# Optimization experiments

Hardware: AMD Instinct MI355X
Metric: run time of the kernel (lower is better)

## Reference

```python
import jax, jax.numpy as jnp
import numpy as np

SEG_SIZES = list(range(3, 102, 2))   # 50 segment sizes, as in FractalImage.__init__
BETA = 4.0                            # soft-count sigmoid sharpness
EPS = 1e-8
R_CAP = 20                            # max number of radii per segment size


def _segment(x, k):
    # Non-overlapping k x k patches: (B,H,W) -> (B, P, k*k)
    B, H, W = x.shape
    nh, nw = H // k, W // k
    p = x[:, :nh * k, :nw * k].reshape(B, nh, k, nw, k)
    return p.transpose(0, 1, 3, 2, 4).reshape(B, nh * nw, k * k)


def _metric_feats(d, radii):
    # d: (B,P,K2) distances from patch center; radii: (R,)
    soft = jax.nn.sigmoid((radii - d[..., None]) * BETA)   # (B,P,K2,R) soft indicator d<=r
    n = soft.mean(axis=2)                                  # (B,P,R) per-patch filling fraction
    nbar = n.mean(axis=1)                                  # (B,R)
    lx = jnp.log(radii)
    xc = lx - lx.mean()
    slope = (jnp.log(nbar + EPS) * xc).sum(-1) / (xc * xc).sum()
    fd = -slope                                            # (B,) fractal dimension
    m1 = n.mean(axis=1)                                    # (B,R) first moment over patches
    m2 = (n * n).mean(axis=1)                              # (B,R) second moment
    lac = (m2 / (m1 * m1 + EPS)).mean(axis=-1)             # (B,) lacunarity
    return fd, lac


def _features_k(x, k):
    patches = _segment(x, k)                               # (B,P,K2)
    c = k // 2
    center = patches[:, :, c * k + c][..., None]
    di = jnp.abs(patches - center)                         # intensity distance to center
    ii, jj = np.meshgrid(np.arange(k), np.arange(k), indexing='ij')
    dy = jnp.asarray(np.abs(ii - c).reshape(-1), jnp.float32)   # (K2,)
    dx = jnp.asarray(np.abs(jj - c).reshape(-1), jnp.float32)   # (K2,)
    R = int(min(max((k - 1) // 2, 2), R_CAP))
    radii = jnp.arange(1, R + 1, dtype=jnp.float32)
    d_cheb = jnp.maximum(jnp.maximum(dy, dx), di)
    d_euc = jnp.sqrt(dy * dy + dx * dx + di * di)
    d_man = dy + dx + di
    return tuple(_metric_feats(d, radii) for d in (d_cheb, d_euc, d_man))


def _forward(x):
    # one pass per segment size (fixed python loop over 50 static sizes)
    feats = [jax.checkpoint(lambda xx, kk=k: _features_k(xx, kk))(x) for k in SEG_SIZES]
    channels = []
    for m in range(3):  # Chebyshev, Euclidean, Manhattan
        fd = jnp.stack([f[m][0] for f in feats], axis=0)   # (50,B)
        lac = jnp.stack([f[m][1] for f in feats], axis=0)  # (50,B)
        # AssembleChannel: transpose, concat [lac, fd] -> (B,100) -> (B,10,10)
        ch = jnp.concatenate([lac.T, fd.T], axis=1).reshape(-1, 10, 10)
        channels.append(ch)
    # AssembleImage: stack metrics as channels -> (B,10,10,3)
    return jnp.stack(channels, axis=-1)


def setup_inputs() -> dict:
    key = jax.random.key(0)
    x = jax.random.uniform(key, (16, 224, 224), dtype=jnp.float32)
    return {"x": x}


def reference(x):
    return _forward(x)
```

## Files before the change

kernel.cpp:

```cpp
#include <hip/hip_runtime.h>
#include <stdint.h>


#define L2E4f 5.770780163555854f
#define QE4f  0.0183156388887342f

struct Tabs {
  int gpre[51];
  int CH[50];
  int kofseq[50];
  int GT;
  int eoff[18], ecnt[18];
  int moff[18], mcnt[18];
  int pbase;
};

__device__ __constant__ float LXT[20] = {
  0.0f, 0.69314718f, 1.09861229f, 1.38629436f, 1.60943791f,
  1.79175947f, 1.94591015f, 2.07944154f, 2.19722458f, 2.30258509f,
  2.39789527f, 2.48490665f, 2.56494936f, 2.63905733f, 2.70805020f,
  2.77258872f, 2.83321334f, 2.89037176f, 2.94443898f, 2.99573227f};

constexpr float PRt[21] = {1.0f,
  5.45981500e1f, 2.98095799e3f, 1.62754791e5f, 8.88611052e6f, 4.85165195e8f,
  2.64891221e10f, 1.44625706e12f, 7.89629602e13f, 4.31123155e15f, 2.35385267e17f,
  1.28516001e19f, 7.01673591e20f, 3.83100800e22f, 2.09165950e24f, 1.14200739e26f,
  6.23514908e27f, 3.40427605e29f, 1.85867175e31f, 1.01480039e33f, 5.54062238e34f};
constexpr float QRt[21] = {1.0f,
  1.83156389e-2f, 3.35462628e-4f, 6.14421235e-6f, 1.12535175e-7f, 2.06115362e-9f,
  3.77513454e-11f, 6.91440011e-13f, 1.26641655e-14f, 2.31952283e-16f, 4.24835426e-18f,
  7.78113224e-20f, 1.42516408e-21f, 2.61027907e-23f, 4.78089288e-25f, 8.75651076e-27f,
  1.60381089e-28f, 2.93748211e-30f, 5.38018616e-32f, 9.85415469e-34f, 1.80485139e-35f};

__device__ __forceinline__ float wred64(float v) {
#pragma unroll
  for (int off = 32; off > 0; off >>= 1) v += __shfl_xor(v, off, 64);
  return v;
}

__device__ __forceinline__ int csqrt_d(int v) {
  if (v <= 0) return 0;
  int x = (int)sqrtf((float)v);
  while (x * x < v) ++x;
  while (x > 0 && (x - 1) * (x - 1) >= v) --x;
  return x;
}

__global__ __launch_bounds__(256) void build_lists(uint32_t* ws, Tabs tab) {
  const int ci = (int)blockIdx.x >> 1;
  const int metric = (int)blockIdx.x & 1;
  const int c_eff = 8 + ci;
  const int cb = (c_eff < 24) ? c_eff : 24;
  const int Rcl = (c_eff < 20) ? c_eff : 20;
  const int tid = (int)threadIdx.x;

  if (metric == 1) {
    const int t1 = (Rcl + 4 < 24) ? Rcl + 4 : 24;
    const int smax = (t1 < 2 * cb) ? t1 : 2 * cb;
    uint32_t* dst = ws + tab.moff[ci];
    for (int s = tid; s <= smax; s += 256) {
      int off = 0;
      for (int s2 = 0; s2 < s; ++s2)
        off += (s2 == 0) ? 1 : ((s2 <= cb) ? 4 * s2 : ((s2 <= 2 * cb) ? 4 * (2 * cb - s2 + 1) : 0));
      const int lim = (s < cb) ? s : cb;
      for (int iy = -lim; iy <= lim; ++iy) {
        const int v = s - ((iy >= 0) ? iy : -iy);
        if (v > cb) continue;
        const uint32_t hs = ((uint32_t)s << 16) | ((uint32_t)(iy + 32) << 8);
        if (v == 0) dst[off++] = hs | 32u;
        else { dst[off++] = hs | (uint32_t)(-v + 32); dst[off++] = hs | (uint32_t)(v + 32); }
      }
    }
    if (tid == 0) {
      int total = 0;
      for (int s = 0; s <= smax; ++s)
        total += (s == 0) ? 1 : ((s <= cb) ? 4 * s : ((s <= 2 * cb) ? 4 * (2 * cb - s + 1) : 0));
      const uint32_t dummy = (40u << 16) | ((uint32_t)(cb + 32) << 8) | (uint32_t)(cb + 32);
      for (int q = total; q < tab.mcnt[ci]; ++q) dst[q] = dummy;
    }
  } else {
    const int amax = (Rcl + 4 < 24) ? Rcl + 4 : 24;
    const int W = 2 * cb + 1;
    __shared__ int rs[25 * 49];
    __shared__ int abase[26];
    uint32_t* dst = ws + tab.eoff[ci];
    for (int pid = tid; pid < (amax + 1) * W; pid += 256) {
      const int a = pid / W, iy = pid % W - cb;
      const int B = (a + 1) * (a + 1) - iy * iy;
      int len = 0;
      if (B > 0) {
        const int A = a * a - iy * iy;
        const int x0 = csqrt_d(A);
        int x1 = csqrt_d(B); if (x1 > cb + 1) x1 = cb + 1;
        if (x1 > x0) len = (x0 == 0) ? (2 * x1 - 1) : 2 * (x1 - x0);
      }
      rs[pid] = len;
    }
    __syncthreads();
    if (tid <= amax) {
      int acc = 0;
      for (int iyi = 0; iyi < W; ++iyi) { const int L = rs[tid * W + iyi]; rs[tid * W + iyi] = acc; acc += L; }
      abase[tid + 1] = acc;
    }
    __syncthreads();
    if (tid == 0) { abase[0] = 0; for (int a = 1; a <= amax + 1; ++a) abase[a] += abase[a - 1]; }
    __syncthreads();
    for (int pid = tid; pid < (amax + 1) * W; pid += 256) {
      const int a = pid / W, iy = pid % W - cb;
      const int B = (a + 1) * (a + 1) - iy * iy;
      if (B <= 0) continue;
      const int A = a * a - iy * iy;
      const int x0 = csqrt_d(A);
      int x1 = csqrt_d(B); if (x1 > cb + 1) x1 = cb + 1;
      if (x1 <= x0) continue;
      int off = abase[a] + rs[pid];
      const uint32_t hs = ((uint32_t)a << 16) | ((uint32_t)(iy + 32) << 8);
      if (x0 == 0) {
        for (int dx = -(x1 - 1); dx <= x1 - 1; ++dx) dst[off++] = hs | (uint32_t)(dx + 32);
      } else {
        for (int dx = -(x1 - 1); dx <= -x0; ++dx) dst[off++] = hs | (uint32_t)(dx + 32);
        for (int dx = x0; dx <= x1 - 1; ++dx)     dst[off++] = hs | (uint32_t)(dx + 32);
      }
    }
    __syncthreads();
    if (tid == 0) {
      const int total = abase[amax + 1];
      const uint32_t dummy = (40u << 16) | ((uint32_t)(cb + 32) << 8) | (uint32_t)(cb + 32);
      for (int q = total; q < tab.ecnt[ci]; ++q) dst[q] = dummy;
    }
  }
}

template<int MAXR>
__device__ __forceinline__ void subwave_path(
    const float* __restrict__ xb, float (*s_red)[80],
    int k, int c, int nw, int k2, int R, float invk2, float rcpk,
    int pstart, int pend, int ch, int lpl, int wid, int lane) {
  const int LP = 1 << lpl;
  const int grp = lane >> lpl;
  const int l0 = lane & (LP - 1);
  const int gpw = 64 >> lpl;
  const int conc = gpw << 2;
  const int rounds = (ch + conc - 1) / conc;

  for (int it = 0; it < rounds; ++it) {
    const int patch = pstart + it * conc + wid * gpw + grp;
    float av[2][MAXR];
#pragma unroll
    for (int m = 0; m < 2; ++m)
#pragma unroll
      for (int r = 0; r < MAXR; ++r) av[m][r] = 0.0f;

    if (patch < pend) {
      const int ph = patch / nw, pw = patch - ph * nw;
      const float* pb = xb + (ph * k) * 224 + pw * k;
      const float center = pb[c * 224 + c];
      for (int p = l0; p < k2; p += LP) {
        const int i = (int)(((float)p + 0.5f) * rcpk);
        const int j = p - i * k;
        const float dy = fabsf((float)(i - c));
        const float dx = fabsf((float)(j - c));
        const float di = fabsf(pb[i * 224 + j] - center);
        const float dman = dy + dx + di;
        const float deuc = sqrtf(dy * dy + dx * dx + di * di);
        float Ee = __builtin_amdgcn_exp2f(L2E4f * (deuc - 1.0f));
        float Em = __builtin_amdgcn_exp2f(L2E4f * (dman - 1.0f));
#pragma unroll
        for (int r = 0; r < MAXR; ++r) {
          if (r < R) {
            av[0][r] += __builtin_amdgcn_rcpf(1.0f + Ee);
            av[1][r] += __builtin_amdgcn_rcpf(1.0f + Em);
            Ee *= QE4f; Em *= QE4f;
          }
        }
      }
    }
#pragma unroll
    for (int m = 0; m < 2; ++m)
#pragma unroll
      for (int r = 0; r < MAXR; ++r) {
        if (r < R) {
          float t = av[m][r];
          for (int off = LP >> 1; off > 0; off >>= 1) t += __shfl_xor(t, off, 64);
          float n = t * invk2;
          float nn = n * n;
          for (int off = LP; off < 64; off <<= 1) {
            n += __shfl_xor(n, off, 64);
            nn += __shfl_xor(nn, off, 64);
          }
          if (lane == 0) {
            s_red[wid][m * 40 + r * 2] += n;
            s_red[wid][m * 40 + r * 2 + 1] += nn;
          }
        }
      }
  }
}

template<int METRIC>
__device__ __forceinline__ void list_pass_pair(
    const uint32_t* __restrict__ lst, int pairs,
    const float* __restrict__ pb, float center,
    int c, int R, float (&av)[2][20], int lane) {
  uint32_t e0 = lst[lane];
  uint32_t e1 = lst[64 + lane];
  for (int it = 0; it < pairs; ++it) {
    const int iy0 = (int)((e0 >> 8) & 255) - 32, dx0 = (int)(e0 & 255) - 32;
    const int iy1 = (int)((e1 >> 8) & 255) - 32, dx1 = (int)(e1 & 255) - 32;
    const float px0 = pb[(c + iy0) * 224 + (c + dx0)];
    const float px1 = pb[(c + iy1) * 224 + (c + dx1)];
    const int s0 = (int)(e0 >> 16), s1 = (int)(e1 >> 16);
    const int slo = __builtin_amdgcn_readfirstlane(s0);
    const int shi = __builtin_amdgcn_readfirstlane(__shfl(s1, 63));
    uint32_t en0 = 0u, en1 = 0u;
    if (it + 1 < pairs) {
      en0 = lst[(2 * it + 2) * 64 + lane];
      en1 = lst[(2 * it + 3) * 64 + lane];
    }

    const int rlo = (slo - 2 > 1) ? slo - 2 : 1;
    const float di0 = fabsf(px0 - center);
    const float di1 = fabsf(px1 - center);
    float d0, d1;
    if (METRIC == 1) {
      d0 = (float)s0 + di0;
      d1 = (float)s1 + di1;
    } else {
      d0 = sqrtf(fmaf(di0, di0, (float)(iy0 * iy0 + dx0 * dx0)));
      d1 = sqrtf(fmaf(di1, di1, (float)(iy1 * iy1 + dx1 * dx1)));
    }
    const float g0 = __builtin_amdgcn_exp2f(-L2E4f * d0);
    const float g1 = __builtin_amdgcn_exp2f(-L2E4f * d1);
    const float gs = g0 + g1;
    float E0 = __builtin_amdgcn_exp2f(L2E4f * (d0 - (float)rlo));
    float E1 = __builtin_amdgcn_exp2f(L2E4f * (d1 - (float)rlo));
    const bool haveones = (shi + 4 <= R);
    const float hs = haveones
        ? (__builtin_amdgcn_rcpf(g0) + __builtin_amdgcn_rcpf(g1)) : 0.0f;
#pragma unroll
    for (int r = 1; r <= 20; ++r) {
      if (r <= R) {
        if (r < rlo) {
          av[METRIC][r - 1] = fmaf(PRt[r], gs, av[METRIC][r - 1]);
        } else if (r <= shi + 3) {
          av[METRIC][r - 1] += __builtin_amdgcn_rcpf(1.0f + E0)
                             + __builtin_amdgcn_rcpf(1.0f + E1);
          E0 *= QE4f; E1 *= QE4f;
        } else {
          av[METRIC][r - 1] += fmaf(hs, -QRt[r], 2.0f);
        }
      }
    }
    e0 = en0; e1 = en1;
  }
}

__global__ __launch_bounds__(256) void fractal_main(const float* __restrict__ x,
                                                    float* __restrict__ ws, Tabs tab) {
  const int g = (int)blockIdx.x;
  const int b = (int)blockIdx.y;
  int seq = 0;
  while (g >= tab.gpre[seq + 1]) ++seq;
  const int kidx = tab.kofseq[seq];
  const int lc = g - tab.gpre[seq];
  const int k = 3 + 2 * kidx, c = k >> 1, nw = 224 / k;
  const int P = nw * nw, k2 = k * k;
  int R = kidx + 1; if (R < 2) R = 2; if (R > 20) R = 20;
  const float invk2 = 1.0f / (float)k2;
  const float rcpk = 1.0f / (float)k;
  const float* xb = x + b * 50176;
  const int tid = (int)threadIdx.x, wid = tid >> 6, lane = tid & 63;
  const int ch = tab.CH[kidx];
  const int pstart = lc * ch;
  int pend = pstart + ch; if (pend > P) pend = P;

  __shared__ float s_red[4][80];
  for (int t = tid; t < 320; t += 256) (&s_red[0][0])[t] = 0.0f;
  __syncthreads();

  if (kidx <= 6) {
    const int lpl = (kidx <= 2) ? 0 : 2;
    subwave_path<8>(xb, s_red, k, c, nw, k2, R, invk2, rcpk, pstart, pend, ch, lpl, wid, lane);
  } else {
    const int ci = (kidx + 1 <= 24) ? (kidx - 7) : 17;
    const uint32_t* wsu = (const uint32_t*)ws;
    const uint32_t* el = wsu + tab.eoff[ci];
    const uint32_t* ml = wsu + tab.moff[ci];
    const int ep = tab.ecnt[ci] >> 7, mp = tab.mcnt[ci] >> 7;
    for (int patch = pstart + wid; patch < pend; patch += 4) {
      const int ph = patch / nw, pw = patch - ph * nw;
      const float* pb = xb + (ph * k) * 224 + pw * k;
      const float center = pb[c * 224 + c];
      float av[2][20];
#pragma unroll
      for (int m = 0; m < 2; ++m)
#pragma unroll
        for (int r = 0; r < 20; ++r) av[m][r] = 0.0f;

      list_pass_pair<0>(el, ep, pb, center, c, R, av, lane);
      list_pass_pair<1>(ml, mp, pb, center, c, R, av, lane);

#pragma unroll
      for (int m = 0; m < 2; ++m)
#pragma unroll
        for (int r = 0; r < 20; ++r) {
          if (r < R) {
            const float tot = wred64(av[m][r]);
            if (lane == 0) {
              const float n = tot * invk2;
              s_red[wid][m * 40 + r * 2] += n;
              s_red[wid][m * 40 + r * 2 + 1] += n * n;
            }
          }
        }
    }
  }

  __syncthreads();
  float* dst = ws + tab.pbase + ((size_t)b * tab.GT + g) * 80;
  if (tid < 80) dst[tid] = s_red[0][tid] + s_red[1][tid] + s_red[2][tid] + s_red[3][tid];
}

__global__ __launch_bounds__(64) void fractal_final(const float* __restrict__ ws,
                                                    float* __restrict__ out, Tabs tab) {
  const int kb = (int)blockIdx.x;
  const int kidx = kb >> 4, b = kb & 15;
  int seq = 0;
  for (int j = 0; j < 50; ++j) if (tab.kofseq[j] == kidx) seq = j;
  const int g0 = tab.gpre[seq], g1 = tab.gpre[seq + 1];
  const int k = 3 + 2 * kidx, c = k >> 1, nw = 224 / k;
  const int P = nw * nw, k2 = k * k;
  int R = kidx + 1; if (R < 2) R = 2; if (R > 20) R = 20;
  const float invP = 1.0f / (float)P;
  const int lane = (int)threadIdx.x;

  float lmean = 0.0f;
  for (int r0 = 0; r0 < 20; ++r0) if (r0 < R) lmean += LXT[r0];
  lmean /= (float)R;
  float sxx = 0.0f;
  for (int r0 = 0; r0 < 20; ++r0)
    if (r0 < R) { const float xc = LXT[r0] - lmean; sxx += xc * xc; }

  __shared__ float s_lac[64], s_sxy[64];
  float lact = 0.0f, sxyt = 0.0f;
  if (lane < 60) {
    const int mo = lane / 20;
    const int r0 = lane % 20, rr = r0 + 1;
    if (rr <= R) {
      float m1, m2;
      if (mo == 0) {
        int s0 = rr - 3; if (s0 > c) s0 = c;
        float acc = (s0 >= 0) ? (1.0f + 4.0f * (float)(s0 * (s0 + 1))) : 0.0f;
        int slo = rr - 2; if (slo < 0) slo = 0;
        int shi = rr + 3; if (shi > c) shi = c;
        for (int s = slo; s <= shi; ++s) {
          const float w = (s == 0) ? 1.0f : 8.0f * (float)s;
          acc += w * __builtin_amdgcn_rcpf(
                   1.0f + __builtin_amdgcn_exp2f(L2E4f * (float)(s - rr)));
        }
        m1 = acc / (float)k2;
        m2 = m1 * m1;
      } else {
        const int mws = mo - 1;
        float sn = 0.0f, sn2 = 0.0f;
        for (int gg = g0; gg < g1; ++gg) {
          const float* p = ws + tab.pbase + ((size_t)b * tab.GT + gg) * 80 + mws * 40 + r0 * 2;
          sn += p[0]; sn2 += p[1];
        }
        m1 = sn * invP; m2 = sn2 * invP;
      }
      lact = m2 / (m1 * m1 + 1e-8f);
      sxyt = logf(m1 + 1e-8f) * (LXT[r0] - lmean);
    }
  }
  s_lac[lane] = lact; s_sxy[lane] = sxyt;
  __syncthreads();
  if (lane < 3) {
    float L = 0.0f, S = 0.0f;
    for (int r0 = 0; r0 < 20; ++r0) { L += s_lac[lane * 20 + r0]; S += s_sxy[lane * 20 + r0]; }
    out[b * 300 + kidx * 3 + lane] = L / (float)R;
    out[b * 300 + (50 + kidx) * 3 + lane] = -S / sxx;
  }
}

static inline int csqrt_h(int v) {
  if (v <= 0) return 0;
  int x = 0;
  while (x * x < v) ++x;
  return x;
}

extern "C" void kernel_launch(void* const* d_in, const int* in_sizes, int n_in,
                              void* d_out, int out_size, void* d_ws, size_t ws_size,
                              hipStream_t stream) {
  Tabs tab;

  int lw = 0;
  for (int ci = 0; ci < 18; ++ci) {
    const int c_eff = 8 + ci;
    const int cb = (c_eff < 24) ? c_eff : 24;
    const int Rcl = (c_eff < 20) ? c_eff : 20;
    const int amax = (Rcl + 4 < 24) ? Rcl + 4 : 24;
    const int t1 = (Rcl + 4 < 24) ? Rcl + 4 : 24;
    const int smax = (t1 < 2 * cb) ? t1 : 2 * cb;
    int ec = 0;
    for (int a = 0; a <= amax; ++a)
      for (int iy = -cb; iy <= cb; ++iy) {
        const int B = (a + 1) * (a + 1) - iy * iy;
        if (B <= 0) continue;
        const int A = a * a - iy * iy;
        const int x0 = csqrt_h(A);
        int x1 = csqrt_h(B); if (x1 > cb + 1) x1 = cb + 1;
        if (x1 > x0) ec += (x0 == 0) ? (2 * x1 - 1) : 2 * (x1 - x0);
      }
    int mc = 0;
    for (int s = 0; s <= smax; ++s)
      mc += (s == 0) ? 1 : ((s <= cb) ? 4 * s : ((s <= 2 * cb) ? 4 * (2 * cb - s + 1) : 0));
    const int ecp = (ec + 127) & ~127;
    const int mcp = (mc + 127) & ~127;
    tab.eoff[ci] = lw; tab.ecnt[ci] = ecp; lw += ecp;
    tab.moff[ci] = lw; tab.mcnt[ci] = mcp; lw += mcp;
  }
  tab.pbase = lw;
  const long budget = (long)ws_size - 4L * lw;

  long T = 10000;
  int G_[50], CH_[50];
  long bc[50];
  for (int tries = 0; tries < 8; ++tries) {
    long GTl = 0;
    for (int i = 0; i < 50; ++i) {
      const int k = 3 + 2 * i, nw = 224 / k, P = nw * nw, k2 = k * k;
      int R = i + 1; if (R < 2) R = 2; if (R > 20) R = 20;
      if (i <= 6) {
        const int lpl = (i <= 2) ? 0 : 2;
        const int LP = 1 << lpl, conc = 256 >> lpl;
        const long rc = (long)((k2 + LP - 1) / LP) * 2L * (12L * R + 8L);
        long np = T / rc; if (np < 1) np = 1;
        long cht = np * conc; if (cht > P) cht = P;
        int G = (int)(((long)P + cht - 1) / cht);
        int ch = (P + G - 1) / G; G = (P + ch - 1) / ch;
        G_[i] = G; CH_[i] = ch;
        bc[i] = (long)((ch + conc - 1) / conc) * rc;
      } else {
        const int ci = (i + 1 <= 24) ? (i - 7) : 17;
        const long trips = (long)((tab.ecnt[ci] + tab.mcnt[ci]) >> 6);
        const long ppc = trips * 340 + 1100;
        long nppb = T / ppc; if (nppb < 4) nppb = 4;
        int cht = (int)(((nppb + 3) / 4) * 4); if (cht > P) cht = P;
        int G = (P + cht - 1) / cht;
        int ch = (P + G - 1) / G; G = (P + ch - 1) / ch;
        G_[i] = G; CH_[i] = ch;
        bc[i] = (long)((ch + 3) / 4) * ppc;
      }
      GTl += G_[i];
    }
    if (16L * GTl * 80L * 4L <= budget || tries == 7) break;
    T *= 2;
  }
  int ord[50];
  for (int i = 0; i < 50; ++i) ord[i] = i;
  for (int a = 1; a < 50; ++a) {
    const int key = ord[a]; const long kw = bc[key];
    int bp = a - 1;
    while (bp >= 0 && bc[ord[bp]] < kw) { ord[bp + 1] = ord[bp]; --bp; }
    ord[bp + 1] = key;
  }
  tab.gpre[0] = 0;
  for (int j = 0; j < 50; ++j) {
    tab.kofseq[j] = ord[j];
    tab.gpre[j + 1] = tab.gpre[j] + G_[ord[j]];
  }
  for (int i = 0; i < 50; ++i) tab.CH[i] = CH_[i];
  tab.GT = tab.gpre[50];

  const float* x = (const float*)d_in[0];
  build_lists<<<36, 256, 0, stream>>>((uint32_t*)d_ws, tab);
  fractal_main<<<dim3(tab.GT, 16), 256, 0, stream>>>(x, (float*)d_ws, tab);
  fractal_final<<<800, 64, 0, stream>>>((const float*)d_ws, (float*)d_out, tab);
}
```

Measured before the change: 185.5 us.

## Process two patches per wave in list pass to amortize offset decode

The list-driven path for larger segment sizes now has each wave handle two adjacent patches at once. Offset decode, list loads and readfirstlane work are shared, and there is twice the independent transcendental work for latency hiding. The transition window is narrowed by one radius (rlo uses slo-1, the exact band ends at shi+2), so fewer exact sigmoid evaluations are done. The host work-cost model and chunk rounding are retuned for the 8-patch-per-block stride. Register pressure rises with two accumulator arrays, and the narrower band may change accuracy.

```diff
diff --git a/kernel.cpp b/kernel.cpp
--- a/kernel.cpp
+++ b/kernel.cpp
@@ -198,17 +198,20 @@
 }
 
 template<int METRIC>
-__device__ __forceinline__ void list_pass_pair(
+__device__ __forceinline__ void list_pass_dual(
     const uint32_t* __restrict__ lst, int pairs,
-    const float* __restrict__ pb, float center,
-    int c, int R, float (&av)[2][20], int lane) {
+    const float* __restrict__ pbA, float cenA,
+    const float* __restrict__ pbB, float cenB,
+    int c, int R, float (&avA)[20], float (&avB)[20], int lane) {
   uint32_t e0 = lst[lane];
   uint32_t e1 = lst[64 + lane];
   for (int it = 0; it < pairs; ++it) {
     const int iy0 = (int)((e0 >> 8) & 255) - 32, dx0 = (int)(e0 & 255) - 32;
     const int iy1 = (int)((e1 >> 8) & 255) - 32, dx1 = (int)(e1 & 255) - 32;
-    const float px0 = pb[(c + iy0) * 224 + (c + dx0)];
-    const float px1 = pb[(c + iy1) * 224 + (c + dx1)];
+    const int off0 = (c + iy0) * 224 + (c + dx0);
+    const int off1 = (c + iy1) * 224 + (c + dx1);
+    const float pA0 = pbA[off0], pA1 = pbA[off1];
+    const float pB0 = pbB[off0], pB1 = pbB[off1];
     const int s0 = (int)(e0 >> 16), s1 = (int)(e1 >> 16);
     const int slo = __builtin_amdgcn_readfirstlane(s0);
     const int shi = __builtin_amdgcn_readfirstlane(__shfl(s1, 63));
@@ -218,36 +221,49 @@
       en1 = lst[(2 * it + 3) * 64 + lane];
     }
 
-    const int rlo = (slo - 2 > 1) ? slo - 2 : 1;
-    const float di0 = fabsf(px0 - center);
-    const float di1 = fabsf(px1 - center);
-    float d0, d1;
+    const int rlo = (slo - 1 > 1) ? slo - 1 : 1;
+    const float diA0 = fabsf(pA0 - cenA), diA1 = fabsf(pA1 - cenA);
+    const float diB0 = fabsf(pB0 - cenB), diB1 = fabsf(pB1 - cenB);
+    float dA0, dA1, dB0, dB1;
     if (METRIC == 1) {
-      d0 = (float)s0 + di0;
-      d1 = (float)s1 + di1;
+      dA0 = (float)s0 + diA0; dA1 = (float)s1 + diA1;
+      dB0 = (float)s0 + diB0; dB1 = (float)s1 + diB1;
     } else {
-      d0 = sqrtf(fmaf(di0, di0, (float)(iy0 * iy0 + dx0 * dx0)));
-      d1 = sqrtf(fmaf(di1, di1, (float)(iy1 * iy1 + dx1 * dx1)));
-    }
-    const float g0 = __builtin_amdgcn_exp2f(-L2E4f * d0);
-    const float g1 = __builtin_amdgcn_exp2f(-L2E4f * d1);
-    const float gs = g0 + g1;
-    float E0 = __builtin_amdgcn_exp2f(L2E4f * (d0 - (float)rlo));
-    float E1 = __builtin_amdgcn_exp2f(L2E4f * (d1 - (float)rlo));
-    const bool haveones = (shi + 4 <= R);
-    const float hs = haveones
-        ? (__builtin_amdgcn_rcpf(g0) + __builtin_amdgcn_rcpf(g1)) : 0.0f;
+      const float rho0 = (float)(iy0 * iy0 + dx0 * dx0);
+      const float rho1 = (float)(iy1 * iy1 + dx1 * dx1);
+      dA0 = sqrtf(fmaf(diA0, diA0, rho0)); dA1 = sqrtf(fmaf(diA1, diA1, rho1));
+      dB0 = sqrtf(fmaf(diB0, diB0, rho0)); dB1 = sqrtf(fmaf(diB1, diB1, rho1));
+    }
+    const float gA0 = __builtin_amdgcn_exp2f(-L2E4f * dA0);
+    const float gA1 = __builtin_amdgcn_exp2f(-L2E4f * dA1);
+    const float gB0 = __builtin_amdgcn_exp2f(-L2E4f * dB0);
+    const float gB1 = __builtin_amdgcn_exp2f(-L2E4f * dB1);
+    const float gsA = gA0 + gA1, gsB = gB0 + gB1;
+    float EA0 = __builtin_amdgcn_exp2f(L2E4f * (dA0 - (float)rlo));
+    float EA1 = __builtin_amdgcn_exp2f(L2E4f * (dA1 - (float)rlo));
+    float EB0 = __builtin_amdgcn_exp2f(L2E4f * (dB0 - (float)rlo));
+    float EB1 = __builtin_amdgcn_exp2f(L2E4f * (dB1 - (float)rlo));
+    const bool haveones = (shi + 3 <= R);
+    float hsA = 0.0f, hsB = 0.0f;
+    if (haveones) {
+      hsA = __builtin_amdgcn_rcpf(gA0) + __builtin_amdgcn_rcpf(gA1);
+      hsB = __builtin_amdgcn_rcpf(gB0) + __builtin_amdgcn_rcpf(gB1);
+    }
 #pragma unroll
     for (int r = 1; r <= 20; ++r) {
       if (r <= R) {
         if (r < rlo) {
-          av[METRIC][r - 1] = fmaf(PRt[r], gs, av[METRIC][r - 1]);
-        } else if (r <= shi + 3) {
-          av[METRIC][r - 1] += __builtin_amdgcn_rcpf(1.0f + E0)
-                             + __builtin_amdgcn_rcpf(1.0f + E1);
-          E0 *= QE4f; E1 *= QE4f;
+          avA[r - 1] = fmaf(PRt[r], gsA, avA[r - 1]);
+          avB[r - 1] = fmaf(PRt[r], gsB, avB[r - 1]);
+        } else if (r <= shi + 2) {
+          avA[r - 1] += __builtin_amdgcn_rcpf(1.0f + EA0)
+                      + __builtin_amdgcn_rcpf(1.0f + EA1);
+          avB[r - 1] += __builtin_amdgcn_rcpf(1.0f + EB0)
+                      + __builtin_amdgcn_rcpf(1.0f + EB1);
+          EA0 *= QE4f; EA1 *= QE4f; EB0 *= QE4f; EB1 *= QE4f;
         } else {
-          av[METRIC][r - 1] += fmaf(hs, -QRt[r], 2.0f);
+          avA[r - 1] += fmaf(hsA, -QRt[r], 2.0f);
+          avB[r - 1] += fmaf(hsB, -QRt[r], 2.0f);
         }
       }
     }
@@ -287,32 +303,57 @@
     const uint32_t* el = wsu + tab.eoff[ci];
     const uint32_t* ml = wsu + tab.moff[ci];
     const int ep = tab.ecnt[ci] >> 7, mp = tab.mcnt[ci] >> 7;
-    for (int patch = pstart + wid; patch < pend; patch += 4) {
-      const int ph = patch / nw, pw = patch - ph * nw;
-      const float* pb = xb + (ph * k) * 224 + pw * k;
-      const float center = pb[c * 224 + c];
-      float av[2][20];
-#pragma unroll
-      for (int m = 0; m < 2; ++m)
-#pragma unroll
-        for (int r = 0; r < 20; ++r) av[m][r] = 0.0f;
-
-      list_pass_pair<0>(el, ep, pb, center, c, R, av, lane);
-      list_pass_pair<1>(ml, mp, pb, center, c, R, av, lane);
-
-#pragma unroll
-      for (int m = 0; m < 2; ++m)
-#pragma unroll
-        for (int r = 0; r < 20; ++r) {
-          if (r < R) {
-            const float tot = wred64(av[m][r]);
-            if (lane == 0) {
-              const float n = tot * invk2;
-              s_red[wid][m * 40 + r * 2] += n;
-              s_red[wid][m * 40 + r * 2 + 1] += n * n;
+    for (int patch = pstart + wid * 2; patch < pend; patch += 8) {
+      const bool hasB = (patch + 1 < pend);
+      const int pbi = hasB ? patch + 1 : patch;
+      const int phA = patch / nw, pwA = patch - phA * nw;
+      const int phB = pbi / nw,  pwB = pbi - phB * nw;
+      const float* pbA = xb + (phA * k) * 224 + pwA * k;
+      const float* pbB = xb + (phB * k) * 224 + pwB * k;
+      const float cenA = pbA[c * 224 + c];
+      const float cenB = pbB[c * 224 + c];
+
+      float avA[20], avB[20];
+#pragma unroll
+      for (int r = 0; r < 20; ++r) { avA[r] = 0.0f; avB[r] = 0.0f; }
+      list_pass_dual<0>(el, ep, pbA, cenA, pbB, cenB, c, R, avA, avB, lane);
+#pragma unroll
+      for (int r = 0; r < 20; ++r) {
+        if (r < R) {
+          const float ta = wred64(avA[r]);
+          const float tb = wred64(avB[r]);
+          if (lane == 0) {
+            const float na = ta * invk2;
+            s_red[wid][r * 2] += na;
+            s_red[wid][r * 2 + 1] += na * na;
+            if (hasB) {
+              const float nb = tb * invk2;
+              s_red[wid][r * 2] += nb;
+              s_red[wid][r * 2 + 1] += nb * nb;
             }
           }
         }
+      }
+#pragma unroll
+      for (int r = 0; r < 20; ++r) { avA[r] = 0.0f; avB[r] = 0.0f; }
+      list_pass_dual<1>(ml, mp, pbA, cenA, pbB, cenB, c, R, avA, avB, lane);
+#pragma unroll
+      for (int r = 0; r < 20; ++r) {
+        if (r < R) {
+          const float ta = wred64(avA[r]);
+          const float tb = wred64(avB[r]);
+          if (lane == 0) {
+            const float na = ta * invk2;
+            s_red[wid][40 + r * 2] += na;
+            s_red[wid][40 + r * 2 + 1] += na * na;
+            if (hasB) {
+              const float nb = tb * invk2;
+              s_red[wid][40 + r * 2] += nb;
+              s_red[wid][40 + r * 2 + 1] += nb * nb;
+            }
+          }
+        }
+      }
     }
   }
 
@@ -445,13 +486,13 @@
       } else {
         const int ci = (i + 1 <= 24) ? (i - 7) : 17;
         const long trips = (long)((tab.ecnt[ci] + tab.mcnt[ci]) >> 6);
-        const long ppc = trips * 340 + 1100;
-        long nppb = T / ppc; if (nppb < 4) nppb = 4;
-        int cht = (int)(((nppb + 3) / 4) * 4); if (cht > P) cht = P;
+        const long ppc = trips * 250 + 1100;
+        long nppb = T / ppc; if (nppb < 8) nppb = 8;
+        int cht = (int)(((nppb + 7) / 8) * 8); if (cht > P) cht = P;
         int G = (P + cht - 1) / cht;
         int ch = (P + G - 1) / G; G = (P + ch - 1) / ch;
         G_[i] = G; CH_[i] = ch;
-        bc[i] = (long)((ch + 3) / 4) * ppc;
+        bc[i] = (long)((ch + 7) / 8) * ppc * 2;
       }
       GTl += G_[i];
     }
```

After: 476.2 us. 157% more time.
